# Kernel tuning notes

Measured on AMD Instinct MI355X. Metric: run time of the kernel, lower is better.

## Reference

```python
import jax, jax.numpy as jnp
import numpy as np

PARTS = [list(range(0, 17)), list(range(17, 22)), list(range(22, 27)),
         list(range(27, 36)), list(range(36, 42)), list(range(42, 48)),
         list(range(48, 68))]
NUM_PARTS = len(PARTS)
V_JOINTS = max(max(p) for p in PARTS) + 1  # 68
# joint -> part index (same as get_corr_joints)
JOINTS = np.zeros((V_JOINTS,), dtype=np.int32)
for j, part in enumerate(PARTS):
    for i in part:
        JOINTS[i] = j
BN_EPS = 1e-5


def setup_inputs() -> dict:
    key = jax.random.key(0)
    k0, k1, k2 = jax.random.split(key, 3)
    N, C, T, V = 512, 1024, 1, V_JOINTS
    x = jax.random.normal(k0, (N, C, T, V), dtype=jnp.float32)
    conv1_w = jax.random.normal(k1, (C // 4, C), dtype=jnp.float32) * 0.02  # 1x1 conv C->C/4
    conv1_b = jnp.zeros((C // 4,), dtype=jnp.float32)
    conv2_w = jax.random.normal(k2, (2,), dtype=jnp.float32) * 0.5  # 1x1 conv 2->1
    conv2_b = jnp.zeros((), dtype=jnp.float32)
    bn_gamma = jnp.ones((C,), dtype=jnp.float32)
    bn_beta = jnp.zeros((C,), dtype=jnp.float32)
    return {"x": x, "conv1_w": conv1_w, "conv1_b": conv1_b,
            "conv2_w": conv2_w, "conv2_b": conv2_b,
            "bn_gamma": bn_gamma, "bn_beta": bn_beta}


def _forward(x, conv1_w, conv1_b, conv2_w, conv2_b, bn_gamma, bn_beta):
    N, C, T, V = x.shape  # T must be 1 (required by original .view)
    joints = jnp.asarray(JOINTS)
    P = NUM_PARTS
    # part-wise mean pool over joints: (V,P) normalized one-hot
    M = jax.nn.one_hot(joints, P, dtype=x.dtype)
    M = M / jnp.sum(M, axis=0, keepdims=True)
    x_parts = jnp.einsum('nctv,vp->nctp', x, M)            # (N,C,T,P)
    # conv1: 1x1, C -> C/4
    h = jnp.einsum('nctp,oc->notp', x_parts, conv1_w) + conv1_b[None, :, None, None]
    x_cap = jnp.mean(h, axis=1, keepdims=True)             # channel avg pool
    x_cmp = jnp.max(h, axis=1, keepdims=True)              # channel max pool
    # conv2: 1x1, 2 -> 1 (cat order is (avg, max))
    att = conv2_w[0] * x_cap + conv2_w[1] * x_cmp + conv2_b  # (N,1,T,P)
    att = jnp.broadcast_to(att, (N, C, T, P)).reshape(N, C, P)
    att = jax.nn.softmax(att, axis=-1)                     # softmax over parts
    # scatter part attention back to joints
    att_j = att[:, :, joints][:, :, None, :]               # (N,C,1,V)
    y = x * att_j
    # BatchNorm2d (training mode: batch stats over N,T,V per channel)
    mean = jnp.mean(y, axis=(0, 2, 3), keepdims=True)
    var = jnp.var(y, axis=(0, 2, 3), keepdims=True)
    y_bn = (y - mean) * jax.lax.rsqrt(var + BN_EPS)
    y_bn = y_bn * bn_gamma[None, :, None, None] + bn_beta[None, :, None, None]
    return jax.nn.relu(y_bn + x)


def reference(x, conv1_w, conv1_b, conv2_w, conv2_b, bn_gamma, bn_beta):
    return _forward(x, conv1_w, conv1_b, conv2_w, conv2_b, bn_gamma, bn_beta)
```

## Files before the change

### kernel.cpp

```cpp
#include <hip/hip_runtime.h>

#define NN 512
#define CC 1024
#define OO 256
#define VV 68
#define PP 7
#define NC (NN*CC)
#define NV_CNT 34816.0f

__device__ __forceinline__ int part_of(int v){
  return (v>=17)+(v>=22)+(v>=27)+(v>=36)+(v>=42)+(v>=48);
}

__global__ __launch_bounds__(256) void k0_repack(const float* __restrict__ w1,
    float* __restrict__ w1p){
  int g = blockIdx.x*256 + threadIdx.x;
  int o = g >> 8, cb = g & 255;
  float4 v = ((const float4*)w1)[g];
  ((float4*)w1p)[cb*256 + o] = v;
}

__global__ __launch_bounds__(256) void k1_partsum(const float* __restrict__ x,
    float* __restrict__ S, float* __restrict__ S2){
  int r = blockIdx.x*256 + threadIdx.x;
  const float4* xr = (const float4*)(x + (size_t)r*VV);
  float s[PP], q[PP];
  #pragma unroll
  for (int p=0;p<PP;p++){ s[p]=0.f; q[p]=0.f; }
  #pragma unroll
  for (int i=0;i<17;i++){
    float4 v4 = xr[i];
    #pragma unroll
    for (int j=0;j<4;j++){
      int p = part_of(i*4+j);
      float e = (j==0)?v4.x:(j==1)?v4.y:(j==2)?v4.z:v4.w;
      s[p] += e;
      q[p] = fmaf(e, e, q[p]);
    }
  }
  #pragma unroll
  for (int p=0;p<PP;p++){
    S [p*NC + r] = s[p];
    S2[p*NC + r] = q[p];
  }
}

__global__ __launch_bounds__(256) void k2_att(const float* __restrict__ S,
    const float* __restrict__ w1p, const float* __restrict__ b1,
    const float* __restrict__ w2, const float* __restrict__ b2,
    float* __restrict__ att){
  int n = blockIdx.x;
  int t = threadIdx.x;
  int oh = t & 31, ch = t >> 5;

  __shared__ float4 sf[PP*256];
  for (int u = t; u < PP*256; u += 256){
    int p = u >> 8, cb = u & 255;
    sf[u] = *(const float4*)(S + (size_t)p*NC + (size_t)n*CC + cb*4);
  }
  __syncthreads();

  float acc[8][PP];
  #pragma unroll
  for (int k=0;k<8;k++)
    #pragma unroll
    for (int p=0;p<PP;p++) acc[k][p] = 0.f;

  const float4* wp = (const float4*)w1p;
  for (int i=0;i<32;i++){
    int gcb = ch*32 + i;
    const float4* wrow = wp + (size_t)gcb*256 + oh;
    float4 w[8];
    #pragma unroll
    for (int k=0;k<8;k++) w[k] = wrow[32*k];
    #pragma unroll
    for (int p=0;p<PP;p++){
      float4 sv = sf[p*256 + gcb];
      #pragma unroll
      for (int k=0;k<8;k++){
        acc[k][p] = fmaf(w[k].x, sv.x, acc[k][p]);
        acc[k][p] = fmaf(w[k].y, sv.y, acc[k][p]);
        acc[k][p] = fmaf(w[k].z, sv.z, acc[k][p]);
        acc[k][p] = fmaf(w[k].w, sv.w, acc[k][p]);
      }
    }
  }

  const float inv_cnt[PP] = {1.f/17.f,1.f/5.f,1.f/5.f,1.f/9.f,1.f/6.f,1.f/6.f,1.f/20.f};
  float* sfl = (float*)sf;
  float bo = b1[t];
  float h[PP];
  #pragma unroll
  for (int p=0;p<PP;p++){
    __syncthreads();
    #pragma unroll
    for (int k=0;k<8;k++) sfl[ch*256 + k*32 + oh] = acc[k][p];
    __syncthreads();
    float hs = 0.f;
    #pragma unroll
    for (int c8=0;c8<8;c8++) hs += sfl[c8*256 + t];
    h[p] = fmaf(hs, inv_cnt[p], bo);
  }

  __shared__ float red_s[4][PP];
  __shared__ float red_m[4][PP];
  __shared__ float pre[PP];
  int lane = t & 63, wid = t >> 6;
  #pragma unroll
  for (int p=0;p<PP;p++){
    float sm = h[p], mx = h[p];
    #pragma unroll
    for (int off=32; off>0; off>>=1){
      sm += __shfl_down(sm, off, 64);
      mx = fmaxf(mx, __shfl_down(mx, off, 64));
    }
    if (lane==0){ red_s[wid][p]=sm; red_m[wid][p]=mx; }
  }
  __syncthreads();
  if (t < PP){
    int p = t;
    float sm = red_s[0][p]+red_s[1][p]+red_s[2][p]+red_s[3][p];
    float mx = fmaxf(fmaxf(red_m[0][p],red_m[1][p]),
                     fmaxf(red_m[2][p],red_m[3][p]));
    pre[p] = w2[0]*(sm*(1.f/(float)OO)) + w2[1]*mx + b2[0];
  }
  __syncthreads();
  if (t == 0){
    float m = pre[0];
    #pragma unroll
    for (int p=1;p<PP;p++) m = fmaxf(m, pre[p]);
    float e[PP], sum=0.f;
    #pragma unroll
    for (int p=0;p<PP;p++){ e[p] = expf(pre[p]-m); sum += e[p]; }
    float inv = 1.f/sum;
    #pragma unroll
    for (int p=0;p<PP;p++) att[n*PP+p] = e[p]*inv;
  }
}

__global__ __launch_bounds__(256) void k3_stats(const float* __restrict__ S,
    const float* __restrict__ S2, const float* __restrict__ att,
    float* __restrict__ partial){
  int cb  = blockIdx.x & 3;
  int nch = blockIdx.x >> 2;
  int c = cb*256 + threadIdx.x;
  float sm=0.f, sq=0.f;
  for (int i=0;i<4;i++){
    int n = nch*4 + i;
    #pragma unroll
    for (int p=0;p<PP;p++){
      float a = att[n*PP+p];
      sm = fmaf(a,   S [p*NC + n*CC + c], sm);
      sq = fmaf(a*a, S2[p*NC + n*CC + c], sq);
    }
  }
  partial[nch*2*CC + c]      = sm;
  partial[nch*2*CC + CC + c] = sq;
}

__global__ __launch_bounds__(256) void k3b_finalize(const float* __restrict__ partial,
    const float* __restrict__ gamma, const float* __restrict__ beta,
    float* __restrict__ scsh){
  int c = blockIdx.x*256 + threadIdx.x;
  float sm=0.f, sq=0.f;
  for (int ch=0;ch<128;ch++){
    sm += partial[ch*2*CC + c];
    sq += partial[ch*2*CC + CC + c];
  }
  float mean = sm * (1.0f/NV_CNT);
  float msq  = sq * (1.0f/NV_CNT);
  float var  = msq - mean*mean;
  float rstd = rsqrtf(var + 1e-5f);
  float sc = gamma[c]*rstd;
  scsh[c]      = sc;
  scsh[CC + c] = beta[c] - mean*sc;
}

__global__ __launch_bounds__(256) void k4_out(const float* __restrict__ x,
    const float* __restrict__ att, const float* __restrict__ scsh,
    float* __restrict__ out){
  int f = blockIdx.x*256 + threadIdx.x;
  int n = blockIdx.x / 68;
  __shared__ float s_att[PP];
  if (threadIdx.x < PP) s_att[threadIdx.x] = att[n*PP + threadIdx.x];
  __syncthreads();
  int r = f/17;
  int q = f - r*17;
  int v0 = q*4;
  int c = r & (CC-1);
  float4 xv = ((const float4*)x)[f];
  float sc = scsh[c];
  float sh = scsh[CC + c];
  float vals[4];
  #pragma unroll
  for (int j=0;j<4;j++){
    int p = part_of(v0 + j);
    float a = s_att[p];
    float e = (j==0)?xv.x:(j==1)?xv.y:(j==2)?xv.z:xv.w;
    vals[j] = fmaxf(fmaf(e, fmaf(a, sc, 1.0f), sh), 0.0f);
  }
  float4 ov; ov.x=vals[0]; ov.y=vals[1]; ov.z=vals[2]; ov.w=vals[3];
  ((float4*)out)[f] = ov;
}

extern "C" void kernel_launch(void* const* d_in, const int* in_sizes, int n_in,
                              void* d_out, int out_size, void* d_ws, size_t ws_size,
                              hipStream_t stream) {
  const float* x     = (const float*)d_in[0];
  const float* w1    = (const float*)d_in[1];
  const float* b1    = (const float*)d_in[2];
  const float* w2    = (const float*)d_in[3];
  const float* b2    = (const float*)d_in[4];
  const float* gamma = (const float*)d_in[5];
  const float* beta  = (const float*)d_in[6];
  float* out = (float*)d_out;

  float* S       = (float*)d_ws;
  float* S2      = S  + 7*NC;
  float* att     = S2 + 7*NC;
  float* partial = att + NN*PP;
  float* scsh    = partial + 128*2*CC;
  float* w1p     = scsh + 2*CC;

  k0_repack   <<<256,         256, 0, stream>>>(w1, w1p);
  k1_partsum  <<<NC/256,      256, 0, stream>>>(x, S, S2);
  k2_att      <<<NN,          256, 0, stream>>>(S, w1p, b1, w2, b2, att);
  k3_stats    <<<512,         256, 0, stream>>>(S, S2, att, partial);
  k3b_finalize<<<CC/256,      256, 0, stream>>>(partial, gamma, beta, scsh);
  k4_out      <<<(NC*17)/256, 256, 0, stream>>>(x, att, scsh, out);
}
```

Measured before the change: 344.2 us.

## Fuse part-sum, attention, and BN stats into one kernel with atomics

The part-sum pass is merged into the attention kernel, so each block reads its x slab directly and keeps part sums in shared memory and squared sums in registers. Per-channel BN statistics are computed in the same kernel and accumulated with atomicAdd into 4 striped buffers. The finalize step moves into the output kernel. This removes the S/S2 round trips through global memory and three launches. The cost is 512 blocks with about 36KB of shared memory each, which limits occupancy while reading x. The atomic accumulation is also order-nondeterministic.

```diff
diff --git a/kernel.cpp b/kernel.cpp
--- a/kernel.cpp
+++ b/kernel.cpp
@@ -12,61 +12,64 @@
   return (v>=17)+(v>=22)+(v>=27)+(v>=36)+(v>=42)+(v>=48);
 }
 
-__global__ __launch_bounds__(256) void k0_repack(const float* __restrict__ w1,
-    float* __restrict__ w1p){
+__global__ __launch_bounds__(256) void k0_prep(const float* __restrict__ w1,
+    float* __restrict__ w1p, float* __restrict__ accum){
   int g = blockIdx.x*256 + threadIdx.x;
   int o = g >> 8, cb = g & 255;
   float4 v = ((const float4*)w1)[g];
   ((float4*)w1p)[cb*256 + o] = v;
-}
-
-__global__ __launch_bounds__(256) void k1_partsum(const float* __restrict__ x,
-    float* __restrict__ S, float* __restrict__ S2){
-  int r = blockIdx.x*256 + threadIdx.x;
-  const float4* xr = (const float4*)(x + (size_t)r*VV);
-  float s[PP], q[PP];
-  #pragma unroll
-  for (int p=0;p<PP;p++){ s[p]=0.f; q[p]=0.f; }
-  #pragma unroll
-  for (int i=0;i<17;i++){
-    float4 v4 = xr[i];
-    #pragma unroll
-    for (int j=0;j<4;j++){
-      int p = part_of(i*4+j);
-      float e = (j==0)?v4.x:(j==1)?v4.y:(j==2)?v4.z:v4.w;
-      s[p] += e;
-      q[p] = fmaf(e, e, q[p]);
-    }
-  }
-  #pragma unroll
-  for (int p=0;p<PP;p++){
-    S [p*NC + r] = s[p];
-    S2[p*NC + r] = q[p];
-  }
-}
-
-__global__ __launch_bounds__(256) void k2_att(const float* __restrict__ S,
+  if (blockIdx.x == 0){
+    float4 z = make_float4(0.f,0.f,0.f,0.f);
+    #pragma unroll
+    for (int i=0;i<8;i++)
+      ((float4*)accum)[i*256 + threadIdx.x] = z;
+  }
+}
+
+__global__ __launch_bounds__(256) void k12_att(const float* __restrict__ x,
     const float* __restrict__ w1p, const float* __restrict__ b1,
     const float* __restrict__ w2, const float* __restrict__ b2,
-    float* __restrict__ att){
+    float* __restrict__ att, float* __restrict__ accum){
   int n = blockIdx.x;
   int t = threadIdx.x;
+
+  __shared__ float sS[PP*1024];
+  __shared__ float hred[8*256];
+  __shared__ float red_s[4][PP], red_m[4][PP], pre[PP], att_s[PP];
+
+  float qreg[4][PP];
+  #pragma unroll
+  for (int j=0;j<4;j++){
+    int c = j*256 + t;
+    const float4* xr = (const float4*)(x + ((size_t)n*CC + c)*VV);
+    float s[PP];
+    #pragma unroll
+    for (int p=0;p<PP;p++){ s[p]=0.f; qreg[j][p]=0.f; }
+    #pragma unroll
+    for (int i=0;i<17;i++){
+      float4 v4 = xr[i];
+      #pragma unroll
+      for (int jj=0;jj<4;jj++){
+        int p = part_of(i*4+jj);
+        float e = (jj==0)?v4.x:(jj==1)?v4.y:(jj==2)?v4.z:v4.w;
+        s[p] += e;
+        qreg[j][p] = fmaf(e, e, qreg[j][p]);
+      }
+    }
+    #pragma unroll
+    for (int p=0;p<PP;p++) sS[p*1024 + c] = s[p];
+  }
+  __syncthreads();
+
   int oh = t & 31, ch = t >> 5;
-
-  __shared__ float4 sf[PP*256];
-  for (int u = t; u < PP*256; u += 256){
-    int p = u >> 8, cb = u & 255;
-    sf[u] = *(const float4*)(S + (size_t)p*NC + (size_t)n*CC + cb*4);
-  }
-  __syncthreads();
-
   float acc[8][PP];
   #pragma unroll
   for (int k=0;k<8;k++)
     #pragma unroll
     for (int p=0;p<PP;p++) acc[k][p] = 0.f;
 
-  const float4* wp = (const float4*)w1p;
+  const float4* wp  = (const float4*)w1p;
+  const float4* sf4 = (const float4*)sS;
   for (int i=0;i<32;i++){
     int gcb = ch*32 + i;
     const float4* wrow = wp + (size_t)gcb*256 + oh;
@@ -75,7 +78,7 @@
     for (int k=0;k<8;k++) w[k] = wrow[32*k];
     #pragma unroll
     for (int p=0;p<PP;p++){
-      float4 sv = sf[p*256 + gcb];
+      float4 sv = sf4[p*256 + gcb];
       #pragma unroll
       for (int k=0;k<8;k++){
         acc[k][p] = fmaf(w[k].x, sv.x, acc[k][p]);
@@ -87,24 +90,20 @@
   }
 
   const float inv_cnt[PP] = {1.f/17.f,1.f/5.f,1.f/5.f,1.f/9.f,1.f/6.f,1.f/6.f,1.f/20.f};
-  float* sfl = (float*)sf;
   float bo = b1[t];
   float h[PP];
   #pragma unroll
   for (int p=0;p<PP;p++){
     __syncthreads();
     #pragma unroll
-    for (int k=0;k<8;k++) sfl[ch*256 + k*32 + oh] = acc[k][p];
+    for (int k=0;k<8;k++) hred[ch*256 + k*32 + oh] = acc[k][p];
     __syncthreads();
     float hs = 0.f;
     #pragma unroll
-    for (int c8=0;c8<8;c8++) hs += sfl[c8*256 + t];
+    for (int c8=0;c8<8;c8++) hs += hred[c8*256 + t];
     h[p] = fmaf(hs, inv_cnt[p], bo);
   }
 
-  __shared__ float red_s[4][PP];
-  __shared__ float red_m[4][PP];
-  __shared__ float pre[PP];
   int lane = t & 63, wid = t >> 6;
   #pragma unroll
   for (int p=0;p<PP;p++){
@@ -134,50 +133,36 @@
     for (int p=0;p<PP;p++){ e[p] = expf(pre[p]-m); sum += e[p]; }
     float inv = 1.f/sum;
     #pragma unroll
-    for (int p=0;p<PP;p++) att[n*PP+p] = e[p]*inv;
-  }
-}
-
-__global__ __launch_bounds__(256) void k3_stats(const float* __restrict__ S,
-    const float* __restrict__ S2, const float* __restrict__ att,
-    float* __restrict__ partial){
-  int cb  = blockIdx.x & 3;
-  int nch = blockIdx.x >> 2;
-  int c = cb*256 + threadIdx.x;
-  float sm=0.f, sq=0.f;
-  for (int i=0;i<4;i++){
-    int n = nch*4 + i;
-    #pragma unroll
     for (int p=0;p<PP;p++){
-      float a = att[n*PP+p];
-      sm = fmaf(a,   S [p*NC + n*CC + c], sm);
-      sq = fmaf(a*a, S2[p*NC + n*CC + c], sq);
-    }
-  }
-  partial[nch*2*CC + c]      = sm;
-  partial[nch*2*CC + CC + c] = sq;
-}
-
-__global__ __launch_bounds__(256) void k3b_finalize(const float* __restrict__ partial,
+      float a = e[p]*inv;
+      att_s[p] = a;
+      att[n*PP+p] = a;
+    }
+  }
+  __syncthreads();
+
+  float a[PP], a2[PP];
+  #pragma unroll
+  for (int p=0;p<PP;p++){ a[p] = att_s[p]; a2[p] = a[p]*a[p]; }
+  float* acc_sm = accum + (n & 3)*2048;
+  float* acc_sq = acc_sm + 1024;
+  #pragma unroll
+  for (int j=0;j<4;j++){
+    int c = j*256 + t;
+    float sm=0.f, sq=0.f;
+    #pragma unroll
+    for (int p=0;p<PP;p++){
+      sm = fmaf(a[p],  sS[p*1024 + c], sm);
+      sq = fmaf(a2[p], qreg[j][p],     sq);
+    }
+    atomicAdd(&acc_sm[c], sm);
+    atomicAdd(&acc_sq[c], sq);
+  }
+}
+
+__global__ __launch_bounds__(256) void k4_out(const float* __restrict__ x,
+    const float* __restrict__ att, const float* __restrict__ accum,
     const float* __restrict__ gamma, const float* __restrict__ beta,
-    float* __restrict__ scsh){
-  int c = blockIdx.x*256 + threadIdx.x;
-  float sm=0.f, sq=0.f;
-  for (int ch=0;ch<128;ch++){
-    sm += partial[ch*2*CC + c];
-    sq += partial[ch*2*CC + CC + c];
-  }
-  float mean = sm * (1.0f/NV_CNT);
-  float msq  = sq * (1.0f/NV_CNT);
-  float var  = msq - mean*mean;
-  float rstd = rsqrtf(var + 1e-5f);
-  float sc = gamma[c]*rstd;
-  scsh[c]      = sc;
-  scsh[CC + c] = beta[c] - mean*sc;
-}
-
-__global__ __launch_bounds__(256) void k4_out(const float* __restrict__ x,
-    const float* __restrict__ att, const float* __restrict__ scsh,
     float* __restrict__ out){
   int f = blockIdx.x*256 + threadIdx.x;
   int n = blockIdx.x / 68;
@@ -189,8 +174,13 @@
   int v0 = q*4;
   int c = r & (CC-1);
   float4 xv = ((const float4*)x)[f];
-  float sc = scsh[c];
-  float sh = scsh[CC + c];
+  float sm = accum[c]      + accum[2048+c] + accum[4096+c] + accum[6144+c];
+  float sq = accum[1024+c] + accum[3072+c] + accum[5120+c] + accum[7168+c];
+  float mean = sm * (1.0f/NV_CNT);
+  float var  = sq * (1.0f/NV_CNT) - mean*mean;
+  float rstd = rsqrtf(var + 1e-5f);
+  float sc = gamma[c]*rstd;
+  float sh = beta[c] - mean*sc;
   float vals[4];
   #pragma unroll
   for (int j=0;j<4;j++){
@@ -215,17 +205,11 @@
   const float* beta  = (const float*)d_in[6];
   float* out = (float*)d_out;
 
-  float* S       = (float*)d_ws;
-  float* S2      = S  + 7*NC;
-  float* att     = S2 + 7*NC;
-  float* partial = att + NN*PP;
-  float* scsh    = partial + 128*2*CC;
-  float* w1p     = scsh + 2*CC;
-
-  k0_repack   <<<256,         256, 0, stream>>>(w1, w1p);
-  k1_partsum  <<<NC/256,      256, 0, stream>>>(x, S, S2);
-  k2_att      <<<NN,          256, 0, stream>>>(S, w1p, b1, w2, b2, att);
-  k3_stats    <<<512,         256, 0, stream>>>(S, S2, att, partial);
-  k3b_finalize<<<CC/256,      256, 0, stream>>>(partial, gamma, beta, scsh);
-  k4_out      <<<(NC*17)/256, 256, 0, stream>>>(x, att, scsh, out);
-}
+  float* w1p   = (float*)d_ws;
+  float* accum = w1p + OO*CC;
+  float* att   = accum + 8192;
+
+  k0_prep <<<256,         256, 0, stream>>>(w1, w1p, accum);
+  k12_att <<<NN,          256, 0, stream>>>(x, w1p, b1, w2, b2, att, accum);
+  k4_out  <<<(NC*17)/256, 256, 0, stream>>>(x, att, accum, gamma, beta, out);
+}
```

Result: slower. 381.2 us (+10.7%).
